# Optimization experiments

Hardware: AMD Instinct MI355X
Metric: run time of the kernel (lower is better)

Reference implementation:

```python
import jax, jax.numpy as jnp
import numpy as np

RADIUS = 8
NUM = 200
EPS = 1e-8


def _conv2d(x, k, pad_mode):
    # x: [B,1,H,W], k: [kh,kw]; same-size conv with given numpy-style padding mode
    ph, pw = k.shape[0] // 2, k.shape[1] // 2
    xp = jnp.pad(x, ((0, 0), (0, 0), (ph, ph), (pw, pw)), mode=pad_mode)
    return jax.lax.conv_general_dilated(
        xp, k[None, None], (1, 1), 'VALID',
        dimension_numbers=('NCHW', 'OIHW', 'NCHW'))


def _gauss_kernel7():
    xs = np.arange(7, dtype=np.float32) - 3.0
    g = np.exp(-0.5 * xs ** 2)
    g /= g.sum()
    return jnp.asarray(np.outer(g, g))


def get_corners(imgs):
    B, _, H, W = imgs.shape
    # kornia rgb_to_grayscale
    gray = 0.299 * imgs[:, 0:1] + 0.587 * imgs[:, 1:2] + 0.114 * imgs[:, 2:3]
    # kornia CornerGFTT: sobel gradients (normalized), gaussian-smoothed structure tensor, min eigenvalue
    sob = jnp.array([[-1., 0., 1.], [-2., 0., 2.], [-1., 0., 1.]], jnp.float32) / 8.0
    dx = _conv2d(gray, sob, 'edge')
    dy = _conv2d(gray, sob.T, 'edge')
    g = _gauss_kernel7()
    dx2 = _conv2d(dx * dx, g, 'reflect')
    dy2 = _conv2d(dy * dy, g, 'reflect')
    dxy = _conv2d(dx * dy, g, 'reflect')
    tr = dx2 + dy2
    det = dx2 * dy2 - dxy * dxy
    resp = 0.5 * (tr - jnp.sqrt(jnp.abs(tr * tr - 4.0 * det)))  # GFTT score (min eigval)
    # kornia nms2d with 5x5 window: keep local maxima
    mp = jax.lax.reduce_window(resp, -jnp.inf, jax.lax.max,
                               (1, 1, 5, 5), (1, 1, 1, 1),
                               [(0, 0), (0, 0), (2, 2), (2, 2)])
    resp = jnp.where(resp == mp, resp, 0.0)
    # unfold/mask/fold with kernel=stride=RADIUS == per non-overlapping 8x8 block:
    # keep elements equal to the block max and > 0
    r = RADIUS
    blk = resp.reshape(B, 1, H // r, r, W // r, r)
    bmax = blk.max(axis=(3, 5), keepdims=True)
    blk = jnp.where((blk > 0) & (blk == bmax), blk, 0.0)
    corners = blk.reshape(B, H * W)
    # top-200 scatter then binarize
    vals, idx = jax.lax.top_k(corners, NUM)
    out = jnp.zeros_like(corners).at[jnp.arange(B)[:, None], idx].set(vals)
    return (out > 0).astype(imgs.dtype).reshape(B, 1, H, W)


def setup_inputs() -> dict:
    key = jax.random.key(0)
    k1, k2, k3, k4 = jax.random.split(key, 4)
    B, N, D, H, W = 16, 2048, 256, 384, 384
    return {
        'descriptors': jax.random.normal(k1, (B, N, D), jnp.float32),
        'scores': jax.random.uniform(k2, (B, N), jnp.float32),
        'scores_dense': jax.random.normal(k3, (B, 1, H, W), jnp.float32),
        'imgs': jax.random.uniform(k4, (B, 3, H, W), jnp.float32),
    }


def reference(descriptors, scores, scores_dense, imgs):
    corners = get_corners(imgs)
    # all-pairs cosine similarity within each batch: pcos[b,i,j]
    norms = jnp.linalg.norm(descriptors, axis=-1)  # [B,N]
    dots = jnp.einsum('bnd,bmd->bnm', descriptors, descriptors)
    pcos = dots / jnp.maximum(norms[:, :, None] * norms[:, None, :], EPS)
    # BCEWithLogitsLoss(scores_dense, corners), mean reduction
    bce = jnp.mean(jnp.logaddexp(0.0, scores_dense) - scores_dense * corners)
    return bce + jnp.mean(jax.nn.relu(pcos))
```

## Files before the change

### kernel.cpp

```cpp
#include <hip/hip_runtime.h>

#define H 384
#define W 384
#define HWSZ (H * W)
#define NB 16
#define ND 2048
#define DD 256

#define OFF_RESP  256
#define OFF_CVAL  9437440
#define OFF_CPOS  9584896
#define OFF_DESCB 9732352
#define OFF_INV   26509568
#define OFF_PSOFT 26640640
#define OFF_PGEMM 26643200
#define OFF_PCORN 26652160
#define OFF_CNT   26652224

__device__ __forceinline__ int clampi(int v) { return v < 0 ? 0 : (v > 383 ? 383 : v); }
__device__ __forceinline__ int refl(int v) { return v < 0 ? -v : (v >= 384 ? 766 - v : v); }

__device__ __forceinline__ unsigned f2e4m3(float x) {
  float a = fabsf(x);
  unsigned s = (__float_as_uint(x) >> 31) << 7;
  if (a >= 448.f) return s | 0x7E;
  if (a < 0.015625f) {
    int m = (int)rintf(a * 512.f);
    return s | (unsigned)m;
  }
  unsigned u = __float_as_uint(a);
  u += 0x7FFFF + ((u >> 20) & 1);
  unsigned e = (u >> 23) - 120;
  unsigned m = (u >> 20) & 7;
  return s | (e << 3) | m;
}

typedef float f32x4 __attribute__((ext_vector_type(4)));

__device__ __forceinline__ void load_lds16(const void* g, void* l) {
  __builtin_amdgcn_global_load_lds((const __attribute__((address_space(1))) void*)g,
                                   (__attribute__((address_space(3))) void*)l, 16, 0, 0);
}

__device__ __forceinline__ void pubf(float* p, float v) {
  __hip_atomic_store(p, v, __ATOMIC_RELAXED, __HIP_MEMORY_SCOPE_AGENT);
}
__device__ __forceinline__ float rdf(const float* p) {
  return __hip_atomic_load(p, __ATOMIC_RELAXED, __HIP_MEMORY_SCOPE_AGENT);
}

__global__ __launch_bounds__(256) void stage1_kernel(const float* __restrict__ imgs,
                                                     float* __restrict__ resp,
                                                     const float* __restrict__ desc,
                                                     unsigned char* __restrict__ descF8,
                                                     float* __restrict__ invn) {
  __shared__ float pbuf[4448];
  __shared__ float ubuf[3648];
  float* p0 = pbuf;
  float* p1 = pbuf + 1482;
  float* p2 = pbuf + 2964;
  float* glf = ubuf;
  float* t0 = ubuf;
  float* t1 = ubuf + 1216;
  float* t2 = ubuf + 2432;

  if (blockIdx.x >= 2304) {
    int wave = threadIdx.x >> 6, lane = threadIdx.x & 63;
    int rbase = (blockIdx.x - 2304) * 32 + wave * 8;
#pragma unroll 2
    for (int it = 0; it < 8; it++) {
      int row = rbase + it;
      const float4* src = (const float4*)(desc + (size_t)row * DD);
      float4 v = src[lane];
      unsigned pk = f2e4m3(v.x) | (f2e4m3(v.y) << 8) | (f2e4m3(v.z) << 16) | (f2e4m3(v.w) << 24);
      ((unsigned*)(descF8 + (size_t)row * DD))[lane] = pk;
      float ss = v.x * v.x + v.y * v.y + v.z * v.z + v.w * v.w;
      for (int off = 32; off; off >>= 1) ss += __shfl_down(ss, off, 64);
      if (lane == 0) invn[row] = 1.f / fmaxf(sqrtf(ss), 1e-4f);
    }
    return;
  }

  const float GW[7] = {0.0044330482f, 0.0540055826f, 0.2420362294f, 0.3990502160f,
                       0.2420362294f, 0.0540055826f, 0.0044330482f};
  int bid = blockIdx.x;
  int b = bid / 144;
  int t = bid % 144;
  int Y0 = (t / 12) * 32, X0 = (t % 12) * 32;
  const float* ib = imgs + (size_t)b * 3 * HWSZ;

  for (int i = threadIdx.x; i < 1600; i += 256) {
    int r = i / 40, c = i % 40;
    int gy = clampi(Y0 - 4 + r), gx = clampi(X0 - 4 + c);
    const float* p = ib + gy * W + gx;
    glf[r * 41 + c] = 0.299f * p[0] + 0.587f * p[HWSZ] + 0.114f * p[2 * HWSZ];
  }
  __syncthreads();

  bool interior = (X0 >= 32 && X0 <= 320 && Y0 >= 32 && Y0 <= 320);

  if (interior) {
    for (int i = threadIdx.x; i < 1444; i += 256) {
      int r = i / 38, c = i % 38;
      const float* g0 = glf + r * 41 + c;
      float a = g0[0],  bb = g0[1],  cc = g0[2];
      float d = g0[41],              e = g0[43];
      float f = g0[82], g = g0[83],  h = g0[84];
      float dx = 0.125f * ((cc - a) + 2.f * (e - d) + (h - f));
      float dy = 0.125f * ((f - a) + 2.f * (g - bb) + (h - cc));
      p0[r * 39 + c] = dx * dx;
      p1[r * 39 + c] = dy * dy;
      p2[r * 39 + c] = dx * dy;
    }
  } else {
    for (int i = threadIdx.x; i < 1444; i += 256) {
      int r = i / 38, c = i % 38;
      int py = refl(Y0 - 3 + r), px = refl(X0 - 3 + c);
      int ym = clampi(py - 1) - (Y0 - 4), y0 = py - (Y0 - 4), yp = clampi(py + 1) - (Y0 - 4);
      int xm = clampi(px - 1) - (X0 - 4), x0 = px - (X0 - 4), xp = clampi(px + 1) - (X0 - 4);
      float a = glf[ym * 41 + xm], bb = glf[ym * 41 + x0], cc = glf[ym * 41 + xp];
      float d = glf[y0 * 41 + xm], e = glf[y0 * 41 + xp];
      float f = glf[yp * 41 + xm], g = glf[yp * 41 + x0], h = glf[yp * 41 + xp];
      float dx = 0.125f * ((cc - a) + 2.f * (e - d) + (h - f));
      float dy = 0.125f * ((f - a) + 2.f * (g - bb) + (h - cc));
      p0[r * 39 + c] = dx * dx;
      p1[r * 39 + c] = dy * dy;
      p2[r * 39 + c] = dx * dy;
    }
  }
  __syncthreads();

  for (int g = threadIdx.x; g < 304; g += 256) {
    int r = g >> 3, c0 = (g & 7) * 4;
    {
      float a[10];
#pragma unroll
      for (int dc = 0; dc < 10; dc++) a[dc] = p0[r * 39 + c0 + dc];
#pragma unroll
      for (int k = 0; k < 4; k++) {
        float sv = 0.f;
#pragma unroll
        for (int j = 0; j < 7; j++) sv += GW[j] * a[k + j];
        t0[r * 32 + c0 + k] = sv;
      }
    }
    {
      float a[10];
#pragma unroll
      for (int dc = 0; dc < 10; dc++) a[dc] = p1[r * 39 + c0 + dc];
#pragma unroll
      for (int k = 0; k < 4; k++) {
        float sv = 0.f;
#pragma unroll
        for (int j = 0; j < 7; j++) sv += GW[j] * a[k + j];
        t1[r * 32 + c0 + k] = sv;
      }
    }
    {
      float a[10];
#pragma unroll
      for (int dc = 0; dc < 10; dc++) a[dc] = p2[r * 39 + c0 + dc];
#pragma unroll
      for (int k = 0; k < 4; k++) {
        float sv = 0.f;
#pragma unroll
        for (int j = 0; j < 7; j++) sv += GW[j] * a[k + j];
        t2[r * 32 + c0 + k] = sv;
      }
    }
  }
  __syncthreads();

  {
    int r0 = (threadIdx.x >> 5) * 4, c = threadIdx.x & 31;
    float s0[4], s1[4], s2[4];
    {
      float a[10];
#pragma unroll
      for (int dr = 0; dr < 10; dr++) a[dr] = t0[(r0 + dr) * 32 + c];
#pragma unroll
      for (int k = 0; k < 4; k++) {
        float sv = 0.f;
#pragma unroll
        for (int j = 0; j < 7; j++) sv += GW[j] * a[k + j];
        s0[k] = sv;
      }
    }
    {
      float a[10];
#pragma unroll
      for (int dr = 0; dr < 10; dr++) a[dr] = t1[(r0 + dr) * 32 + c];
#pragma unroll
      for (int k = 0; k < 4; k++) {
        float sv = 0.f;
#pragma unroll
        for (int j = 0; j < 7; j++) sv += GW[j] * a[k + j];
        s1[k] = sv;
      }
    }
    {
      float a[10];
#pragma unroll
      for (int dr = 0; dr < 10; dr++) a[dr] = t2[(r0 + dr) * 32 + c];
#pragma unroll
      for (int k = 0; k < 4; k++) {
        float sv = 0.f;
#pragma unroll
        for (int j = 0; j < 7; j++) sv += GW[j] * a[k + j];
        s2[k] = sv;
      }
    }
#pragma unroll
    for (int k = 0; k < 4; k++) {
      float tr = s0[k] + s1[k];
      float det = s0[k] * s1[k] - s2[k] * s2[k];
      float disc = tr * tr - 4.f * det;
      float rv = 0.5f * (tr - sqrtf(fabsf(disc)));
      resp[(size_t)b * HWSZ + (Y0 + r0 + k) * W + (X0 + c)] = rv;
    }
  }
}

__global__ __launch_bounds__(256) void stage2_kernel(const float* __restrict__ resp,
                                                     float* __restrict__ cval,
                                                     unsigned* __restrict__ cpos,
                                                     const float4* __restrict__ sd4,
                                                     float* __restrict__ psoft,
                                                     int* __restrict__ cnt) {
  __shared__ float rl[68][37];
  __shared__ float rmx[68][32];
  __shared__ float r4[4];

  if (blockIdx.x >= 1152) {
    int sb = blockIdx.x - 1152;
    if (sb == 0 && threadIdx.x == 0) { cnt[0] = 0; cnt[1] = 0; }
    float s = 0.f;
    int base = sb * 256 + threadIdx.x;
#pragma unroll
    for (int it = 0; it < 4; it++) {
      float4 v = sd4[base + it * 147456];
      s += fmaxf(v.x, 0.f) + log1pf(expf(-fabsf(v.x))) +
           fmaxf(v.y, 0.f) + log1pf(expf(-fabsf(v.y))) +
           fmaxf(v.z, 0.f) + log1pf(expf(-fabsf(v.z))) +
           fmaxf(v.w, 0.f) + log1pf(expf(-fabsf(v.w)));
    }
    for (int off = 32; off; off >>= 1) s += __shfl_down(s, off, 64);
    if ((threadIdx.x & 63) == 0) r4[threadIdx.x >> 6] = s;
    __syncthreads();
    if (threadIdx.x == 0) psoft[sb] = r4[0] + r4[1] + r4[2] + r4[3];
    return;
  }

  int bid = blockIdx.x;
  int b = bid / 72;
  int t = bid % 72;
  int Y0 = (t / 12) * 64, X0 = (t % 12) * 32;
  const float* rb = resp + (size_t)b * HWSZ;

  for (int i = threadIdx.x; i < 68 * 36; i += 256) {
    int r = i / 36, c = i % 36;
    int gy = Y0 - 2 + r, gx = X0 - 2 + c;
    float v = -INFINITY;
    if (gy >= 0 && gy < H && gx >= 0 && gx < W) v = rb[gy * W + gx];
    rl[r][c] = v;
  }
  __syncthreads();

  for (int i = threadIdx.x; i < 68 * 32; i += 256) {
    int r = i / 32, c = i % 32;
    float m = rl[r][c];
    m = fmaxf(m, rl[r][c + 1]);
    m = fmaxf(m, rl[r][c + 2]);
    m = fmaxf(m, rl[r][c + 3]);
    m = fmaxf(m, rl[r][c + 4]);
    rmx[r][c] = m;
  }
  __syncthreads();

  for (int i = threadIdx.x; i < 2048; i += 256) {
    int r = i / 32, c = i % 32;
    float m = rmx[r][c];
    m = fmaxf(m, rmx[r + 1][c]);
    m = fmaxf(m, rmx[r + 2][c]);
    m = fmaxf(m, rmx[r + 3][c]);
    m = fmaxf(m, rmx[r + 4][c]);
    float v = rl[r + 2][c + 2];
    rl[r + 2][c + 2] = (v == m) ? v : 0.f;
  }
  __syncthreads();

  if (threadIdx.x < 32) {
    int bi = threadIdx.x >> 2, bj = threadIdx.x & 3;
    float bv = 0.f;
    unsigned bp = 0;
    for (int rr = 0; rr < 8; rr++)
      for (int cc = 0; cc < 8; cc++) {
        float v = rl[bi * 8 + rr + 2][bj * 8 + cc + 2];
        if (v > bv) { bv = v; bp = (unsigned)((Y0 + bi * 8 + rr) * W + (X0 + bj * 8 + cc)); }
      }
    int ci = b * 2304 + (Y0 / 8 + bi) * 48 + (X0 / 8 + bj);
    cval[ci] = bv;
    cpos[ci] = bp;
  }
}

__global__ __launch_bounds__(256) void stage3_kernel(const float* __restrict__ cval,
                                                     const unsigned* __restrict__ cpos,
                                                     const float* __restrict__ sd,
                                                     float* __restrict__ pcorn,
                                                     const unsigned char* __restrict__ descF8,
                                                     const float* __restrict__ invn,
                                                     float* __restrict__ pgemm,
                                                     const float* __restrict__ psoft,
                                                     int* __restrict__ cnt,
                                                     float* __restrict__ out) {
  alignas(16) __shared__ char smem[32768];
  __shared__ int finFlag;
  int tid = threadIdx.x;

  if (blockIdx.x < 16) {
    int* hist = (int*)smem;
    int* pick = (int*)(smem + 1024);
    int* eqcnt = (int*)(smem + 1032);
    int* ri = (int*)(smem + 1040);
    unsigned* eqpos = (unsigned*)(smem + 1056);
    float* r4 = (float*)(smem + 2080);

    int b = blockIdx.x;
    int t = tid;
    int lane = t & 63;

    unsigned bits[9], pos[9];
#pragma unroll
    for (int q = 0; q < 9; q++) {
      int i = t + q * 256;
      unsigned vb = 0, p = 0;
      if (i < 2304) {
        float v = cval[b * 2304 + i];
        if (v > 0.f) { vb = __float_as_uint(v); p = cpos[b * 2304 + i]; }
      }
      bits[q] = vb; pos[q] = p;
    }

    int P = 0;
#pragma unroll
    for (int q = 0; q < 9; q++) P += (bits[q] != 0u);
    for (int off = 32; off; off >>= 1) P += __shfl_down(P, off, 64);
    if (lane == 0) ri[t >> 6] = P;
    __syncthreads();
    int Ptot = ri[0] + ri[1] + ri[2] + ri[3];

    float total = 0.f;
    if (Ptot > 0) {
      int K = Ptot < 200 ? Ptot : 200;

      unsigned prefix = 0;
      int krem = K;
      for (int shift = 24; shift >= 0; shift -= 8) {
        hist[t] = 0;
        __syncthreads();
#pragma unroll
        for (int q = 0; q < 9; q++) {
          if (bits[q] != 0u &&
              (shift == 24 || (bits[q] >> (shift + 8)) == (prefix >> (shift + 8))))
            atomicAdd(&hist[(bits[q] >> shift) & 0xFF], 1);
        }
        __syncthreads();
        if (t < 64) {
          int h0 = hist[4 * t], h1 = hist[4 * t + 1], h2 = hist[4 * t + 2], h3 = hist[4 * t + 3];
          int tot = h0 + h1 + h2 + h3;
          int acc = tot;
          for (int d = 1; d < 64; d <<= 1) {
            int o = __shfl_down(acc, d, 64);
            if (t + d < 64) acc += o;
          }
          int excl = acc - tot;
          int G3 = excl, G2 = excl + h3, G1 = excl + h3 + h2, G0 = excl + h3 + h2 + h1;
          if (G0 < krem && G0 + h0 >= krem) { pick[0] = 4 * t;     pick[1] = G0; }
          if (G1 < krem && G1 + h1 >= krem) { pick[0] = 4 * t + 1; pick[1] = G1; }
          if (G2 < krem && G2 + h2 >= krem) { pick[0] = 4 * t + 2; pick[1] = G2; }
          if (G3 < krem && G3 + h3 >= krem) { pick[0] = 4 * t + 3; pick[1] = G3; }
        }
        __syncthreads();
        prefix |= ((unsigned)pick[0]) << shift;
        krem -= pick[1];
        __syncthreads();
      }

      if (t == 0) *eqcnt = 0;
      __syncthreads();
      float s = 0.f;
#pragma unroll
      for (int q = 0; q < 9; q++) {
        if (bits[q] > prefix) s += sd[(size_t)b * HWSZ + pos[q]];
        else if (bits[q] != 0u && bits[q] == prefix) {
          int idx = atomicAdd(eqcnt, 1);
          if (idx < 256) eqpos[idx] = pos[q];
        }
      }
      __syncthreads();
      int m = *eqcnt;
      if (m <= krem) {
        if (t < m) s += sd[(size_t)b * HWSZ + eqpos[t]];
      } else {
        int mm = m < 256 ? m : 256;
        if (t < mm) {
          unsigned p = eqpos[t];
          int rank = 0;
          for (int u = 0; u < mm; u++) rank += (eqpos[u] < p);
          if (rank < krem) s += sd[(size_t)b * HWSZ + p];
        }
      }
      for (int off = 32; off; off >>= 1) s += __shfl_down(s, off, 64);
      if (lane == 0) r4[t >> 6] = s;
      __syncthreads();
      total = r4[0] + r4[1] + r4[2] + r4[3];
    }

    if (t == 0) {
      pubf(&pcorn[b], total);
      asm volatile("s_waitcnt vmcnt(0)" ::: "memory");
      int arr = __hip_atomic_fetch_add(&cnt[1], 1, __ATOMIC_RELAXED, __HIP_MEMORY_SCOPE_AGENT);
      finFlag = (arr == 15);
      if (finFlag) {
        while (__hip_atomic_load(&cnt[0], __ATOMIC_RELAXED, __HIP_MEMORY_SCOPE_AGENT) < 2176)
          __builtin_amdgcn_s_sleep(16);
      }
    }
    __syncthreads();
    if (!finFlag) return;

    float bce = 0.f;
    for (int i = t; i < 576; i += 256) bce += psoft[i];
    if (t < 16) bce -= rdf(&pcorn[t]);
    float g = 0.f;
    for (int i = t; i < 2176; i += 256) g += rdf(&pgemm[i]);
    float v = bce * (1.f / 2359296.f) + g * (1.f / 67108864.f);
    for (int off = 32; off; off >>= 1) v += __shfl_down(v, off, 64);
    if (lane == 0) r4[t >> 6] = v;
    __syncthreads();
    if (t == 0) out[0] = r4[0] + r4[1] + r4[2] + r4[3];
    return;
  }

  char* lA = smem;
  char* lB = smem + 16384;

  int bxl = blockIdx.x - 16;
  int bx = ((bxl & 7) * 272) + (bxl >> 3);
  int batch = bx / 136;
  int rem = bx % 136;
  int ti = 0, rowlen = 16;
  while (rem >= rowlen) { rem -= rowlen; rowlen--; ti++; }
  int tj = ti + rem;

  const unsigned char* Ab = descF8 + (size_t)batch * ND * DD;
  const float* inv = invn + batch * ND;
  int I0 = ti * 128, J0 = tj * 128;

  int wave = tid >> 6, lane = tid & 63;
  int rm = lane & 15, kq = lane >> 4;
  int wr = wave >> 1, wc = wave & 1;
  int lrow = lane >> 3;
  int lcolb = ((lane & 7) ^ lrow) << 4;
  int cx = rm & 7;

  f32x4 accf[4][4];
#pragma unroll
  for (int m = 0; m < 4; m++)
#pragma unroll
    for (int n = 0; n < 4; n++) accf[m][n] = (f32x4){0.f, 0.f, 0.f, 0.f};

  for (int k0 = 0; k0 < DD; k0 += 128) {
#pragma unroll
    for (int q = 0; q < 4; q++) {
      int chunk = wave * 4 + q;
      load_lds16(Ab + (size_t)(I0 + chunk * 8 + lrow) * DD + k0 + lcolb, lA + chunk * 1024);
      load_lds16(Ab + (size_t)(J0 + chunk * 8 + lrow) * DD + k0 + lcolb, lB + chunk * 1024);
    }
    __syncthreads();
#pragma unroll
    for (int kk = 0; kk < 128; kk += 32) {
      long af[4], bfr[4];
      int koff = kk + kq * 8;
      int pcol = ((((koff >> 4) ^ cx) << 4) | (koff & 8));
#pragma unroll
      for (int m = 0; m < 4; m++)
        af[m] = *reinterpret_cast<const long*>(lA + (wr * 64 + m * 16 + rm) * 128 + pcol);
#pragma unroll
      for (int n = 0; n < 4; n++)
        bfr[n] = *reinterpret_cast<const long*>(lB + (wc * 64 + n * 16 + rm) * 128 + pcol);
#pragma unroll
      for (int m = 0; m < 4; m++)
#pragma unroll
        for (int n = 0; n < 4; n++)
          accf[m][n] = __builtin_amdgcn_mfma_f32_16x16x32_fp8_fp8(af[m], bfr[n], accf[m][n], 0, 0, 0);
    }
    __syncthreads();
  }

  float wgt = (ti == tj) ? 1.f : 2.f;
  float invC[4];
#pragma unroll
  for (int n = 0; n < 4; n++) invC[n] = inv[J0 + wc * 64 + n * 16 + rm];
  float psum = 0.f;
#pragma unroll
  for (int m = 0; m < 4; m++) {
#pragma unroll
    for (int r = 0; r < 4; r++) {
      float invR = inv[I0 + wr * 64 + m * 16 + kq * 4 + r];
#pragma unroll
      for (int n = 0; n < 4; n++) psum += fmaxf(accf[m][n][r] * invR * invC[n], 0.f);
    }
  }
  psum *= wgt;
  for (int off = 32; off; off >>= 1) psum += __shfl_down(psum, off, 64);
  float* r4 = (float*)smem;
  if (lane == 0) r4[wave] = psum;
  __syncthreads();
  if (tid == 0) {
    pubf(&pgemm[bx], r4[0] + r4[1] + r4[2] + r4[3]);
    asm volatile("s_waitcnt vmcnt(0)" ::: "memory");
    __hip_atomic_fetch_add(&cnt[0], 1, __ATOMIC_RELAXED, __HIP_MEMORY_SCOPE_AGENT);
  }
}

extern "C" void kernel_launch(void* const* d_in, const int* in_sizes, int n_in,
                              void* d_out, int out_size, void* d_ws, size_t ws_size,
                              hipStream_t stream) {
  (void)in_sizes; (void)n_in; (void)out_size; (void)ws_size;
  const float* desc = (const float*)d_in[0];
  const float* sd = (const float*)d_in[2];
  const float* imgs = (const float*)d_in[3];
  float* out = (float*)d_out;

  char* w = (char*)d_ws;
  float* resp = (float*)(w + OFF_RESP);
  float* cval = (float*)(w + OFF_CVAL);
  unsigned* cpos = (unsigned*)(w + OFF_CPOS);
  unsigned char* descF8 = (unsigned char*)(w + OFF_DESCB);
  float* invn = (float*)(w + OFF_INV);
  float* psoft = (float*)(w + OFF_PSOFT);
  float* pgemm = (float*)(w + OFF_PGEMM);
  float* pcorn = (float*)(w + OFF_PCORN);
  int* cnt = (int*)(w + OFF_CNT);

  stage1_kernel<<<3328, 256, 0, stream>>>(imgs, resp, desc, descF8, invn);
  stage2_kernel<<<1728, 256, 0, stream>>>(resp, cval, cpos, (const float4*)sd, psoft, cnt);
  stage3_kernel<<<2192, 256, 0, stream>>>(cval, cpos, sd, pcorn, descF8, invn,
                                          pgemm, psoft, cnt, out);
}
```

Before: 169.4 us.

## Move softplus reduction into stage3, spread conversion rows, shard completion counters

The softplus/BCE partial sums move from stage2 into extra blocks of stage3, and a finisher block waits on their completion. The single completion counter becomes eight counters on separate cache lines to reduce atomic contention. The descriptor FP8 conversion now uses one row per wave across many more stage1 blocks instead of eight rows per wave. This rebalances work across launches and reduces contention, at the cost of more blocks and a longer spin-wait in the final block.

```diff
diff --git a/kernel.cpp b/kernel.cpp
--- a/kernel.cpp
+++ b/kernel.cpp
@@ -66,18 +66,14 @@
 
   if (blockIdx.x >= 2304) {
     int wave = threadIdx.x >> 6, lane = threadIdx.x & 63;
-    int rbase = (blockIdx.x - 2304) * 32 + wave * 8;
-#pragma unroll 2
-    for (int it = 0; it < 8; it++) {
-      int row = rbase + it;
-      const float4* src = (const float4*)(desc + (size_t)row * DD);
-      float4 v = src[lane];
-      unsigned pk = f2e4m3(v.x) | (f2e4m3(v.y) << 8) | (f2e4m3(v.z) << 16) | (f2e4m3(v.w) << 24);
-      ((unsigned*)(descF8 + (size_t)row * DD))[lane] = pk;
-      float ss = v.x * v.x + v.y * v.y + v.z * v.z + v.w * v.w;
-      for (int off = 32; off; off >>= 1) ss += __shfl_down(ss, off, 64);
-      if (lane == 0) invn[row] = 1.f / fmaxf(sqrtf(ss), 1e-4f);
-    }
+    int row = (blockIdx.x - 2304) * 4 + wave;
+    const float4* src = (const float4*)(desc + (size_t)row * DD);
+    float4 v = src[lane];
+    unsigned pk = f2e4m3(v.x) | (f2e4m3(v.y) << 8) | (f2e4m3(v.z) << 16) | (f2e4m3(v.w) << 24);
+    ((unsigned*)(descF8 + (size_t)row * DD))[lane] = pk;
+    float ss = v.x * v.x + v.y * v.y + v.z * v.z + v.w * v.w;
+    for (int off = 32; off; off >>= 1) ss += __shfl_down(ss, off, 64);
+    if (lane == 0) invn[row] = 1.f / fmaxf(sqrtf(ss), 1e-4f);
     return;
   }
 
@@ -224,32 +220,11 @@
 __global__ __launch_bounds__(256) void stage2_kernel(const float* __restrict__ resp,
                                                      float* __restrict__ cval,
                                                      unsigned* __restrict__ cpos,
-                                                     const float4* __restrict__ sd4,
-                                                     float* __restrict__ psoft,
                                                      int* __restrict__ cnt) {
   __shared__ float rl[68][37];
   __shared__ float rmx[68][32];
-  __shared__ float r4[4];
-
-  if (blockIdx.x >= 1152) {
-    int sb = blockIdx.x - 1152;
-    if (sb == 0 && threadIdx.x == 0) { cnt[0] = 0; cnt[1] = 0; }
-    float s = 0.f;
-    int base = sb * 256 + threadIdx.x;
-#pragma unroll
-    for (int it = 0; it < 4; it++) {
-      float4 v = sd4[base + it * 147456];
-      s += fmaxf(v.x, 0.f) + log1pf(expf(-fabsf(v.x))) +
-           fmaxf(v.y, 0.f) + log1pf(expf(-fabsf(v.y))) +
-           fmaxf(v.z, 0.f) + log1pf(expf(-fabsf(v.z))) +
-           fmaxf(v.w, 0.f) + log1pf(expf(-fabsf(v.w)));
-    }
-    for (int off = 32; off; off >>= 1) s += __shfl_down(s, off, 64);
-    if ((threadIdx.x & 63) == 0) r4[threadIdx.x >> 6] = s;
-    __syncthreads();
-    if (threadIdx.x == 0) psoft[sb] = r4[0] + r4[1] + r4[2] + r4[3];
-    return;
-  }
+
+  if (blockIdx.x == 0 && threadIdx.x < 9) cnt[threadIdx.x * 64] = 0;
 
   int bid = blockIdx.x;
   int b = bid / 72;
@@ -311,11 +286,10 @@
                                                      const unsigned char* __restrict__ descF8,
                                                      const float* __restrict__ invn,
                                                      float* __restrict__ pgemm,
-                                                     const float* __restrict__ psoft,
+                                                     float* __restrict__ psoft,
                                                      int* __restrict__ cnt,
                                                      float* __restrict__ out) {
   alignas(16) __shared__ char smem[32768];
-  __shared__ int finFlag;
   int tid = threadIdx.x;
 
   if (blockIdx.x < 16) {
@@ -325,6 +299,7 @@
     int* ri = (int*)(smem + 1040);
     unsigned* eqpos = (unsigned*)(smem + 1056);
     float* r4 = (float*)(smem + 2080);
+    int* finFlag = (int*)(smem + 2096);
 
     int b = blockIdx.x;
     int t = tid;
@@ -420,18 +395,24 @@
     if (t == 0) {
       pubf(&pcorn[b], total);
       asm volatile("s_waitcnt vmcnt(0)" ::: "memory");
-      int arr = __hip_atomic_fetch_add(&cnt[1], 1, __ATOMIC_RELAXED, __HIP_MEMORY_SCOPE_AGENT);
-      finFlag = (arr == 15);
-      if (finFlag) {
-        while (__hip_atomic_load(&cnt[0], __ATOMIC_RELAXED, __HIP_MEMORY_SCOPE_AGENT) < 2176)
+      int arr = __hip_atomic_fetch_add(&cnt[512], 1, __ATOMIC_RELAXED, __HIP_MEMORY_SCOPE_AGENT);
+      *finFlag = (arr == 15);
+      if (arr == 15) {
+        for (;;) {
+          int sall = 0;
+#pragma unroll
+          for (int i = 0; i < 8; i++)
+            sall += __hip_atomic_load(&cnt[i * 64], __ATOMIC_RELAXED, __HIP_MEMORY_SCOPE_AGENT);
+          if (sall >= 2752) break;
           __builtin_amdgcn_s_sleep(16);
+        }
       }
     }
     __syncthreads();
-    if (!finFlag) return;
+    if (!*finFlag) return;
 
     float bce = 0.f;
-    for (int i = t; i < 576; i += 256) bce += psoft[i];
+    for (int i = t; i < 576; i += 256) bce += rdf(&psoft[i]);
     if (t < 16) bce -= rdf(&pcorn[t]);
     float g = 0.f;
     for (int i = t; i < 2176; i += 256) g += rdf(&pgemm[i]);
@@ -443,10 +424,36 @@
     return;
   }
 
+  if (blockIdx.x < 592) {
+    int sb = blockIdx.x - 16;
+    float* r4 = (float*)smem;
+    const float4* sd4 = (const float4*)sd;
+    float s = 0.f;
+    int base = sb * 256 + tid;
+#pragma unroll
+    for (int it = 0; it < 4; it++) {
+      float4 v = sd4[base + it * 147456];
+      s += fmaxf(v.x, 0.f) + log1pf(expf(-fabsf(v.x))) +
+           fmaxf(v.y, 0.f) + log1pf(expf(-fabsf(v.y))) +
+           fmaxf(v.z, 0.f) + log1pf(expf(-fabsf(v.z))) +
+           fmaxf(v.w, 0.f) + log1pf(expf(-fabsf(v.w)));
+    }
+    for (int off = 32; off; off >>= 1) s += __shfl_down(s, off, 64);
+    if ((tid & 63) == 0) r4[tid >> 6] = s;
+    __syncthreads();
+    if (tid == 0) {
+      pubf(&psoft[sb], r4[0] + r4[1] + r4[2] + r4[3]);
+      asm volatile("s_waitcnt vmcnt(0)" ::: "memory");
+      __hip_atomic_fetch_add(&cnt[(blockIdx.x & 7) * 64], 1,
+                             __ATOMIC_RELAXED, __HIP_MEMORY_SCOPE_AGENT);
+    }
+    return;
+  }
+
   char* lA = smem;
   char* lB = smem + 16384;
 
-  int bxl = blockIdx.x - 16;
+  int bxl = blockIdx.x - 592;
   int bx = ((bxl & 7) * 272) + (bxl >> 3);
   int batch = bx / 136;
   int rem = bx % 136;
@@ -521,7 +528,8 @@
   if (tid == 0) {
     pubf(&pgemm[bx], r4[0] + r4[1] + r4[2] + r4[3]);
     asm volatile("s_waitcnt vmcnt(0)" ::: "memory");
-    __hip_atomic_fetch_add(&cnt[0], 1, __ATOMIC_RELAXED, __HIP_MEMORY_SCOPE_AGENT);
+    __hip_atomic_fetch_add(&cnt[(blockIdx.x & 7) * 64], 1,
+                           __ATOMIC_RELAXED, __HIP_MEMORY_SCOPE_AGENT);
   }
 }
 
@@ -545,8 +553,8 @@
   float* pcorn = (float*)(w + OFF_PCORN);
   int* cnt = (int*)(w + OFF_CNT);
 
-  stage1_kernel<<<3328, 256, 0, stream>>>(imgs, resp, desc, descF8, invn);
-  stage2_kernel<<<1728, 256, 0, stream>>>(resp, cval, cpos, (const float4*)sd, psoft, cnt);
-  stage3_kernel<<<2192, 256, 0, stream>>>(cval, cpos, sd, pcorn, descF8, invn,
+  stage1_kernel<<<10496, 256, 0, stream>>>(imgs, resp, desc, descF8, invn);
+  stage2_kernel<<<1152, 256, 0, stream>>>(resp, cval, cpos, cnt);
+  stage3_kernel<<<2768, 256, 0, stream>>>(cval, cpos, sd, pcorn, descF8, invn,
                                           pgemm, psoft, cnt, out);
 }
```

Measured after the change: 159.1 us. 1.06x faster.
